# Optimization experiments

Measured on AMD Instinct MI355X. Metric: run time of the kernel, lower is better.

## Reference

```python
import jax, jax.numpy as jnp
import numpy as np

N, C, H, W = 16, 64, 128, 128
SHIFT = 1  # frozen value of torch module's random.randint(-2, 2) drawn at __init__


def setup_inputs() -> dict:
    key = jax.random.key(0)
    k1, k2, k3 = jax.random.split(key, 3)
    x = jax.random.normal(k1, (N, C, H, W), dtype=jnp.float32)
    # p_3: Conv2d(c, c, (1,5), padding=(0,2), bias=False) -> weight (C_out, C_in, 1, 5)
    w3 = jax.random.normal(k2, (C, C, 1, 5), dtype=jnp.float32) * (1.0 / np.sqrt(5.0 * C))
    # p_7: Conv2d(9c, c, 1, groups=c, bias=False) -> per output channel, 9 input channels: (C, 9)
    w7 = jax.random.normal(k3, (C, 9), dtype=jnp.float32) * (1.0 / 3.0)
    return {"x": x, "w3": w3, "w7": w7}


def reference(x, w3, w7):
    n, c, h, w = x.shape
    # t_1: F.unfold(x, (1,3), dilation=(1,2), padding=(0,2)) -> width offsets -2, 0, +2 (zero padded)
    xp = jnp.pad(x, ((0, 0), (0, 0), (0, 0), (2, 2)))
    t1 = jnp.stack([xp[..., 0:w], xp[..., 2:w + 2], xp[..., 4:w + 4]], axis=2)  # (n,c,3,h,w)
    # t_3: 1x5 conv, padding (0,2)
    t3 = jax.lax.conv_general_dilated(
        x, w3, window_strides=(1, 1), padding=[(0, 0), (2, 2)],
        dimension_numbers=("NCHW", "OIHW", "NCHW"))  # (n,c,h,w)
    # t_4: F.unfold(t1 as (n,3c,h,w), (3,1), padding=(1,0)) -> height offsets -1, 0, +1
    t1p = jnp.pad(t1, ((0, 0), (0, 0), (0, 0), (1, 1), (0, 0)))
    t4 = jnp.stack([t1p[..., 0:h, :], t1p[..., 1:h + 1, :], t1p[..., 2:h + 2, :]],
                   axis=3)  # (n, c, 3[w_off], 3[h_off], h, w)
    # t_5: roll along the W axis (dim 5)
    t5 = jnp.roll(t4, SHIFT, axis=5)
    # t_6: maximum of lhs (n,c,1,3,h,w) and rhs (n,c,3,3,h,w); lhs offset dim aligns with rhs dim 3
    t6 = jnp.maximum(t1[:, :, None, :, :, :], t5)  # (n,c,3,3,h,w)
    # t_7: grouped 1x1 conv, groups=c, 9 input channels per group -> 1 output channel
    t6f = t6.reshape(n, c, 9, h, w)
    t7 = jnp.einsum("nckhw,ck->nchw", t6f, w7)
    return t7 * t3
```

## Files before the change

kernel.cpp:

```cpp
#include <hip/hip_runtime.h>

#define NN 16
#define CC 64
#define HH 128
#define WW 128

#define LDS_STRIDE 72
#define T3B_STRIDE 132

typedef __attribute__((ext_vector_type(8))) short short8;
typedef __attribute__((ext_vector_type(4))) float floatx4;

__device__ __forceinline__ short f2bf(float f) {
    union { float f; unsigned u; } v; v.f = f;
    unsigned r = v.u + 0x7fffu + ((v.u >> 16) & 1u);
    return (short)(r >> 16);
}
__device__ __forceinline__ unsigned pack2bf(float lo, float hi) {
    union { float f; unsigned u; } a, b; a.f = lo; b.f = hi;
    unsigned ra = a.u + 0x7fffu + ((a.u >> 16) & 1u);
    unsigned rb = b.u + 0x7fffu + ((b.u >> 16) & 1u);
    return (ra >> 16) | (rb & 0xffff0000u);
}
__device__ __forceinline__ float bf2f(unsigned short u) {
    union { unsigned u; float f; } v; v.u = ((unsigned)u) << 16;
    return v.f;
}

__global__ __launch_bounds__(256) void prep_w(const float* __restrict__ w3,
                                              short* __restrict__ Abf,
                                              float* __restrict__ zp) {
    int idx = blockIdx.x * 256 + threadIdx.x;
    if (idx < CC * CC * 5) {
        int tap = idx % 5;
        int ci  = (idx / 5) % CC;
        int co  = idx / (5 * CC);
        Abf[co * 320 + tap * 64 + ci] = f2bf(w3[idx]);
    }
    if (blockIdx.x == 0 && threadIdx.x < 64) zp[threadIdx.x] = 0.f;
}

__global__ __launch_bounds__(256, 4) void fused(const float* __restrict__ x,
                                                const short* __restrict__ Abf,
                                                const float* __restrict__ w7,
                                                const float* __restrict__ zp,
                                                float* __restrict__ out) {
    __shared__ __align__(16) char smem[132 * LDS_STRIDE * 2];
    short*    xsT = (short*)smem;
    unsigned* xsW = (unsigned*)smem;
    short*    t3b = (short*)smem;

    const int bid = blockIdx.x;
    const int nh  = ((bid & 7) << 8) | (bid >> 3);
    const int n   = nh >> 7;
    const int h   = nh & (HH - 1);
    const int tid = threadIdx.x;

    const float* xbase = x + (((size_t)n * CC) * HH + h) * WW;
    {
        const int cp  = tid & 31;
        const int wqg = tid >> 5;
        const float* r0 = xbase + (size_t)(2 * cp) * (HH * WW);
        const float* r1 = r0 + HH * WW;
        #pragma unroll
        for (int q = 0; q < 4; ++q) {
            int wq = wqg * 4 + q;
            float4 a = *(const float4*)(r0 + wq * 4);
            float4 b = *(const float4*)(r1 + wq * 4);
            int wp = wq * 4 + 2;
            xsW[(wp + 0) * 36 + cp] = pack2bf(a.x, b.x);
            xsW[(wp + 1) * 36 + cp] = pack2bf(a.y, b.y);
            xsW[(wp + 2) * 36 + cp] = pack2bf(a.z, b.z);
            xsW[(wp + 3) * 36 + cp] = pack2bf(a.w, b.w);
        }
        if (tid < 128) {
            int wpi = tid >> 5;
            int wpz = (wpi < 2) ? wpi : 128 + wpi;
            xsW[wpz * 36 + (tid & 31)] = 0u;
        }
    }
    __syncthreads();

    const int W    = tid >> 6;
    const int lane = tid & 63;
    const int lm   = lane & 15;
    const int g    = lane >> 4;
    const int mh   = W >> 1;
    const int wh   = W & 1;

    floatx4 acc[2][4];
    #pragma unroll
    for (int m = 0; m < 2; ++m)
        #pragma unroll
        for (int j = 0; j < 4; ++j) acc[m][j] = (floatx4){0.f, 0.f, 0.f, 0.f};

    const short* arow = Abf + (mh * 32 + lm) * 320;

    for (int ks = 0; ks < 10; ++ks) {
        const int kbase = ks * 32 + g * 8;
        const int tap   = kbase >> 6;
        const int cib   = kbase & 63;

        short8 a0 = *(const short8*)(arow + kbase);
        short8 a1 = *(const short8*)(arow + 16 * 320 + kbase);
        #pragma unroll
        for (int j = 0; j < 4; ++j) {
            int wp = (wh * 4 + j) * 16 + lm + tap;
            short8 b = *(const short8*)&xsT[wp * LDS_STRIDE + cib];
            acc[0][j] = __builtin_amdgcn_mfma_f32_16x16x32_bf16(a0, b, acc[0][j], 0, 0, 0);
            acc[1][j] = __builtin_amdgcn_mfma_f32_16x16x32_bf16(a1, b, acc[1][j], 0, 0, 0);
        }
    }
    __syncthreads();

    const int w0  = (tid & 31) * 4;
    const int chi = tid >> 5;
    const bool isw = (w0 == 0);
    const int src  = lane | 31;

    const float* p[9];
    int s[9];
    const float* xb0 = x + (((size_t)(n * CC + chi)) * HH) * WW;
    #pragma unroll
    for (int r = 0; r < 3; ++r) {
        int hh = h + r - 1;
        bool hok = (unsigned)hh < HH;
        #pragma unroll
        for (int q = 0; q < 3; ++q) {
            int cb = w0 - 4 + q * 4;
            bool ok = hok && (unsigned)cb < WW;
            p[r * 3 + q] = ok ? (xb0 + (size_t)hh * WW + cb) : zp;
            s[r * 3 + q] = ok ? (8 * HH * WW) : 0;
        }
    }
    const float* wcp = w7 + chi * 9;
    int t3o = chi * T3B_STRIDE + w0;
    float* outp = out + ((((size_t)(n * CC + chi)) * HH + h) * WW) + w0;

    float4 cur[9];
    #pragma unroll
    for (int t = 0; t < 9; ++t) { cur[t] = *(const float4*)p[t]; p[t] += s[t]; }
    __builtin_amdgcn_sched_barrier(0);

    #pragma unroll
    for (int m = 0; m < 2; ++m)
        #pragma unroll
        for (int j = 0; j < 4; ++j)
            #pragma unroll
            for (int r = 0; r < 4; ++r) {
                int co = (mh * 2 + m) * 16 + g * 4 + r;
                t3b[co * T3B_STRIDE + (wh * 4 + j) * 16 + lm] = f2bf(acc[m][j][r]);
            }

    __syncthreads();

    #pragma unroll
    for (int it = 0; it < 8; ++it) {
        float4 nxt[9];
        if (it < 7) {
            #pragma unroll
            for (int t = 0; t < 9; ++t) { nxt[t] = *(const float4*)p[t]; p[t] += s[t]; }
        }
        float wc[9];
        #pragma unroll
        for (int t = 0; t < 9; ++t) wc[t] = wcp[t];
        ushort4 tv = *(const ushort4*)&t3b[t3o];

        __builtin_amdgcn_sched_barrier(0);

        float win[3][12];
        #pragma unroll
        for (int r = 0; r < 3; ++r) {
            #pragma unroll
            for (int q = 0; q < 3; ++q) {
                float4 v = cur[r * 3 + q];
                win[r][q * 4 + 0] = v.x; win[r][q * 4 + 1] = v.y;
                win[r][q * 4 + 2] = v.z; win[r][q * 4 + 3] = v.w;
            }
        }
        float wrap0[3], wrap1[3];
        #pragma unroll
        for (int r = 0; r < 3; ++r) {
            wrap0[r] = __shfl(win[r][5], src);
            wrap1[r] = __shfl(win[r][7], src);
        }

        float t3v[4] = {bf2f(tv.x), bf2f(tv.y), bf2f(tv.z), bf2f(tv.w)};

        float res[4];
        #pragma unroll
        for (int e = 0; e < 4; ++e) {
            float a = 0.f;
            #pragma unroll
            for (int j = 0; j < 3; ++j) {
                #pragma unroll
                for (int i = 0; i < 3; ++i) {
                    float lhs = win[1][e + 2 * i + 2];
                    float rhs = win[i][e + 2 * j + 1];
                    if (e == 0)
                        rhs = isw ? ((j == 0) ? wrap0[i]
                                   : (j == 1) ? wrap1[i] : 0.f)
                                  : rhs;
                    a = fmaf(wc[j * 3 + i], fmaxf(lhs, rhs), a);
                }
            }
            res[e] = a;
        }
        float4 o;
        o.x = res[0] * t3v[0]; o.y = res[1] * t3v[1];
        o.z = res[2] * t3v[2]; o.w = res[3] * t3v[3];
        *(float4*)outp = o;

        wcp  += 8 * 9;
        t3o  += 8 * T3B_STRIDE;
        outp += (size_t)8 * HH * WW;
        #pragma unroll
        for (int t = 0; t < 9; ++t) cur[t] = nxt[t];
    }
}

extern "C" void kernel_launch(void* const* d_in, const int* in_sizes, int n_in,
                              void* d_out, int out_size, void* d_ws, size_t ws_size,
                              hipStream_t stream) {
    const float* x  = (const float*)d_in[0];
    const float* w3 = (const float*)d_in[1];
    const float* w7 = (const float*)d_in[2];
    float* out = (float*)d_out;

    short* Abf = (short*)d_ws;
    float* zp  = (float*)((char*)d_ws + 40960);

    prep_w<<<(CC * CC * 5 + 255) / 256, 256, 0, stream>>>(w3, Abf, zp);
    fused<<<NN * HH, 256, 0, stream>>>(x, Abf, w7, zp, out);
}
```

Before: 158.3 us.

## Split fused kernel into separate t3 GEMM and combine kernels via output buffer

Splits the single fused kernel into two kernels. The MFMA 1x5-conv GEMM kernel writes t3 as bf16 into the output buffer, using the first half of each output row as scratch. A second combine kernel reads that back, does the shifted max and grouped 1x1 conv, and overwrites the output with floats. This lets the GEMM kernel ask for higher occupancy and frees the combine kernel from the LDS staging and barriers. In exchange it adds a global round trip for t3, an extra kernel launch, and drops the software prefetch of the x window in the combine loop.

```diff
diff --git a/kernel.cpp b/kernel.cpp
--- a/kernel.cpp
+++ b/kernel.cpp
@@ -6,7 +6,6 @@
 #define WW 128
 
 #define LDS_STRIDE 72
-#define T3B_STRIDE 132
 
 typedef __attribute__((ext_vector_type(8))) short short8;
 typedef __attribute__((ext_vector_type(4))) float floatx4;
@@ -40,15 +39,12 @@
     if (blockIdx.x == 0 && threadIdx.x < 64) zp[threadIdx.x] = 0.f;
 }
 
-__global__ __launch_bounds__(256, 4) void fused(const float* __restrict__ x,
-                                                const short* __restrict__ Abf,
-                                                const float* __restrict__ w7,
-                                                const float* __restrict__ zp,
-                                                float* __restrict__ out) {
+__global__ __launch_bounds__(256, 8) void t3gemm(const float* __restrict__ x,
+                                                 const short* __restrict__ Abf,
+                                                 float* __restrict__ out) {
     __shared__ __align__(16) char smem[132 * LDS_STRIDE * 2];
     short*    xsT = (short*)smem;
     unsigned* xsW = (unsigned*)smem;
-    short*    t3b = (short*)smem;
 
     const int bid = blockIdx.x;
     const int nh  = ((bid & 7) << 8) | (bid >> 3);
@@ -81,8 +77,8 @@
     }
     __syncthreads();
 
+    const int lane = tid & 63;
     const int W    = tid >> 6;
-    const int lane = tid & 63;
     const int lm   = lane & 15;
     const int g    = lane >> 4;
     const int mh   = W >> 1;
@@ -111,7 +107,30 @@
             acc[1][j] = __builtin_amdgcn_mfma_f32_16x16x32_bf16(a1, b, acc[1][j], 0, 0, 0);
         }
     }
-    __syncthreads();
+
+    short* t3s = (short*)out;
+    #pragma unroll
+    for (int m = 0; m < 2; ++m)
+        #pragma unroll
+        for (int j = 0; j < 4; ++j)
+            #pragma unroll
+            for (int r = 0; r < 4; ++r) {
+                int co = (mh * 2 + m) * 16 + g * 4 + r;
+                int w  = (wh * 4 + j) * 16 + lm;
+                t3s[((size_t)(n * CC + co) * HH + h) * 256 + w] = f2bf(acc[m][j][r]);
+            }
+}
+
+__global__ __launch_bounds__(256, 4) void combine(const float* __restrict__ x,
+                                                  const float* __restrict__ w7,
+                                                  const float* __restrict__ zp,
+                                                  float* __restrict__ out) {
+    const int bid = blockIdx.x;
+    const int nh  = ((bid & 7) << 8) | (bid >> 3);
+    const int n   = nh >> 7;
+    const int h   = nh & (HH - 1);
+    const int tid = threadIdx.x;
+    const int lane = tid & 63;
 
     const int w0  = (tid & 31) * 4;
     const int chi = tid >> 5;
@@ -134,39 +153,19 @@
         }
     }
     const float* wcp = w7 + chi * 9;
-    int t3o = chi * T3B_STRIDE + w0;
+    const short* t3s = (const short*)out;
+    size_t t3o = ((size_t)(n * CC + chi) * HH + h) * 256 + w0;
     float* outp = out + ((((size_t)(n * CC + chi)) * HH + h) * WW) + w0;
 
-    float4 cur[9];
-    #pragma unroll
-    for (int t = 0; t < 9; ++t) { cur[t] = *(const float4*)p[t]; p[t] += s[t]; }
-    __builtin_amdgcn_sched_barrier(0);
-
-    #pragma unroll
-    for (int m = 0; m < 2; ++m)
-        #pragma unroll
-        for (int j = 0; j < 4; ++j)
-            #pragma unroll
-            for (int r = 0; r < 4; ++r) {
-                int co = (mh * 2 + m) * 16 + g * 4 + r;
-                t3b[co * T3B_STRIDE + (wh * 4 + j) * 16 + lm] = f2bf(acc[m][j][r]);
-            }
-
-    __syncthreads();
-
     #pragma unroll
     for (int it = 0; it < 8; ++it) {
-        float4 nxt[9];
-        if (it < 7) {
-            #pragma unroll
-            for (int t = 0; t < 9; ++t) { nxt[t] = *(const float4*)p[t]; p[t] += s[t]; }
-        }
+        float4 cur[9];
+        #pragma unroll
+        for (int t = 0; t < 9; ++t) { cur[t] = *(const float4*)p[t]; p[t] += s[t]; }
         float wc[9];
         #pragma unroll
         for (int t = 0; t < 9; ++t) wc[t] = wcp[t];
-        ushort4 tv = *(const ushort4*)&t3b[t3o];
-
-        __builtin_amdgcn_sched_barrier(0);
+        ushort4 tv = *(const ushort4*)&t3s[t3o];
 
         float win[3][12];
         #pragma unroll
@@ -212,10 +211,8 @@
         *(float4*)outp = o;
 
         wcp  += 8 * 9;
-        t3o  += 8 * T3B_STRIDE;
+        t3o  += (size_t)8 * HH * 256;
         outp += (size_t)8 * HH * WW;
-        #pragma unroll
-        for (int t = 0; t < 9; ++t) cur[t] = nxt[t];
     }
 }
 
@@ -231,5 +228,6 @@
     float* zp  = (float*)((char*)d_ws + 40960);
 
     prep_w<<<(CC * CC * 5 + 255) / 256, 256, 0, stream>>>(w3, Abf, zp);
-    fused<<<NN * HH, 256, 0, stream>>>(x, Abf, w7, zp, out);
-}
+    t3gemm<<<NN * HH, 256, 0, stream>>>(x, Abf, out);
+    combine<<<NN * HH, 256, 0, stream>>>(x, w7, zp, out);
+}
```

Result: slower. 178.2 us (+12.6%).
